# Kernel optimization log

Hardware: AMD Instinct MI355X
Metric: run time of the kernel (lower is better)

The kernel has to match this reference:

```python
import jax, jax.numpy as jnp
import numpy as np

EPS = 1e-5  # BatchNorm eps (ME.MinkowskiBatchNorm default)


def setup_inputs() -> dict:
    key = jax.random.key(0)
    k1, k2, k3, k4 = jax.random.split(key, 4)
    N, Cin, Cout, K = 65536, 256, 128, 8  # K = kernel_size**dimension = 2**3
    x = jax.random.normal(k1, (N, Cin), dtype=jnp.float32)
    W = jax.random.normal(k2, (K, Cin, Cout), dtype=jnp.float32) * 0.02
    gamma = jax.random.uniform(k3, (Cout,), dtype=jnp.float32, minval=0.5, maxval=1.5)
    beta = jax.random.normal(k4, (Cout,), dtype=jnp.float32) * 0.1
    return {"x": x, "W": W, "gamma": gamma, "beta": beta}


def reference(x, W, gamma, beta):
    # Transpose Minkowski conv, kernel=2, stride=2, dim=3: each input voxel
    # emits 2^3 = 8 disjoint child voxels; child for offset k gets x @ W[k].
    # Kernel map is identity per offset (no scatter-add collisions because
    # kernel_size == stride), so outputs stack to [8*N, Cout].
    Cout = W.shape[-1]
    out = jnp.einsum('nc,kcd->knd', x, W).reshape(-1, Cout)  # [8N, Cout]
    # MinkowskiBatchNorm over all active output sites (training batch stats).
    mean = jnp.mean(out, axis=0)
    var = jnp.mean(jnp.square(out - mean), axis=0)  # biased var, as BN uses
    y = (out - mean) * jax.lax.rsqrt(var + EPS) * gamma + beta
    return jnp.maximum(y, 0.0)  # MinkowskiReLU
```

## Files before the change

kernel.cpp:

```cpp
#include <hip/hip_runtime.h>
#include <stdint.h>

#define N_ROWS 65536
#define CIN 256
#define COUT 128

typedef __bf16 bf16x8 __attribute__((ext_vector_type(8)));
typedef float f32x4 __attribute__((ext_vector_type(4)));
typedef unsigned short u16;
typedef unsigned int u32;

__device__ __forceinline__ float truncbf(float f) {
  u32 x = __builtin_bit_cast(u32, f) & 0xFFFF0000u;
  return __builtin_bit_cast(float, x);
}
__device__ __forceinline__ u32 packbf(float a, float b) {
  return __builtin_amdgcn_perm(__builtin_bit_cast(u32, b),
                               __builtin_bit_cast(u32, a), 0x07060302u);
}

__device__ __forceinline__ void async_ld16(const void* g, void* l) {
  __builtin_amdgcn_global_load_lds((const __attribute__((address_space(1))) u32*)g,
                                   (__attribute__((address_space(3))) u32*)l,
                                   16, 0, 0);
}

template <bool EMIT_XB>
__global__ __launch_bounds__(512, 2) void gram_partial(const float* __restrict__ x,
                                                       float* __restrict__ part,
                                                       float* __restrict__ colsum,
                                                       u32* __restrict__ xb) {
  __shared__ u32 xT[256 * 18];
  __shared__ float cs_s[4][256];
  const int tid = threadIdx.x, lane = tid & 63;
  const int w = tid >> 6;
  const int wm = w >> 2, wn = w & 3;
  const int q = lane >> 4, r = lane & 15;
  const int row0 = blockIdx.x * 256;
  const int cpair = tid & 127, c0 = cpair * 2;
  const int npb = tid >> 7;

  f32x4 acc[8][4];
  #pragma unroll
  for (int i = 0; i < 8; ++i)
    #pragma unroll
    for (int j = 0; j < 4; ++j) acc[i][j] = (f32x4){0.f, 0.f, 0.f, 0.f};
  float cs0 = 0.f, cs1 = 0.f;

  for (int ch = 0; ch < 8; ++ch) {
    const int r0 = row0 + ch * 32;
    #pragma unroll
    for (int i = 0; i < 4; ++i) {
      int np = npb + i * 4;
      int n0 = r0 + np * 2;
      float2 g0 = *(const float2*)&x[(size_t)n0 * CIN + c0];
      float2 g1 = *(const float2*)&x[(size_t)(n0 + 1) * CIN + c0];
      xT[18 * c0 + np] = packbf(g0.x, g1.x);
      xT[18 * (c0 + 1) + np] = packbf(g0.y, g1.y);
      if (EMIT_XB) {
        xb[(size_t)n0 * 128 + cpair] = packbf(g0.x, g0.y);
        xb[(size_t)(n0 + 1) * 128 + cpair] = packbf(g1.x, g1.y);
      }
      cs0 += truncbf(g0.x) + truncbf(g1.x);
      cs1 += truncbf(g0.y) + truncbf(g1.y);
    }
    __syncthreads();
    bf16x8 af[8], bfr[4];
    #pragma unroll
    for (int mt = 0; mt < 8; ++mt) {
      int c = wm * 128 + mt * 16 + r;
      union { u32 d[4]; bf16x8 v; } t;
      const u32* p = &xT[18 * c + 4 * q];
      t.d[0] = p[0]; t.d[1] = p[1]; t.d[2] = p[2]; t.d[3] = p[3];
      af[mt] = t.v;
    }
    #pragma unroll
    for (int nt = 0; nt < 4; ++nt) {
      int c = wn * 64 + nt * 16 + r;
      union { u32 d[4]; bf16x8 v; } t;
      const u32* p = &xT[18 * c + 4 * q];
      t.d[0] = p[0]; t.d[1] = p[1]; t.d[2] = p[2]; t.d[3] = p[3];
      bfr[nt] = t.v;
    }
    #pragma unroll
    for (int mt = 0; mt < 8; ++mt)
      #pragma unroll
      for (int nt = 0; nt < 4; ++nt)
        acc[mt][nt] = __builtin_amdgcn_mfma_f32_16x16x32_bf16(af[mt], bfr[nt], acc[mt][nt], 0, 0, 0);
    __syncthreads();
  }

  float* pb = part + (size_t)blockIdx.x * 65536;
  #pragma unroll
  for (int mt = 0; mt < 8; ++mt)
    #pragma unroll
    for (int nt = 0; nt < 4; ++nt)
      #pragma unroll
      for (int i = 0; i < 4; ++i) {
        int row = wm * 128 + mt * 16 + q * 4 + i;
        int col = wn * 64 + nt * 16 + r;
        pb[row * 256 + col] = acc[mt][nt][i];
      }

  cs_s[npb][c0] = cs0;
  cs_s[npb][c0 + 1] = cs1;
  __syncthreads();
  if (tid < 256)
    atomicAdd(&colsum[tid], cs_s[0][tid] + cs_s[1][tid] + cs_s[2][tid] + cs_s[3][tid]);
}

__global__ void gram_reduce(const float* __restrict__ part, float* __restrict__ G) {
  int g = blockIdx.x * 256 + threadIdx.x;
  float s = 0.f;
  for (int b = 0; b < 256; ++b) s += part[(size_t)b * 65536 + g];
  G[g] = s;
}

__global__ __launch_bounds__(256) void stats_kernel(const float* __restrict__ G,
                                                    const float* __restrict__ colsum,
                                                    const float* __restrict__ W,
                                                    const float* __restrict__ gamma,
                                                    const float* __restrict__ beta,
                                                    float* __restrict__ scale,
                                                    float* __restrict__ bias) {
  const int d = blockIdx.x;
  const int t = threadIdx.x;
  __shared__ float wv[256][8];
  __shared__ float rr[16];
  float wt[8];
  #pragma unroll
  for (int k = 0; k < 8; ++k) wt[k] = truncbf(W[((size_t)k * CIN + t) * COUT + d]);
  #pragma unroll
  for (int k = 0; k < 8; ++k) wv[t][k] = wt[k];
  __syncthreads();

  float q = 0.f;
  for (int j = 0; j < 256; ++j) {
    float g = G[j * 256 + t];
    float dot = 0.f;
    #pragma unroll
    for (int k = 0; k < 8; ++k) dot += wv[j][k] * wt[k];
    q += g * dot;
  }
  float wsum = 0.f;
  #pragma unroll
  for (int k = 0; k < 8; ++k) wsum += wt[k];
  float m = colsum[t] * wsum;

  #pragma unroll
  for (int off = 32; off; off >>= 1) {
    q += __shfl_down(q, off, 64);
    m += __shfl_down(m, off, 64);
  }
  int wid = t >> 6;
  if ((t & 63) == 0) { rr[wid] = q; rr[wid + 8] = m; }
  __syncthreads();
  if (t == 0) {
    float qt = rr[0] + rr[1] + rr[2] + rr[3];
    float mn = rr[8] + rr[9] + rr[10] + rr[11];
    const float invM = 1.f / 524288.f;
    float mean = mn * invM;
    float var = qt * invM - mean * mean;
    float s = gamma[d] * rsqrtf(var + 1e-5f);
    scale[d] = s;
    bias[d] = beta[d] - mean * s;
  }
}

__global__ void wtrans_kernel(const float* __restrict__ W, u16* __restrict__ Wt) {
  __shared__ u16 tile[32][128];
  const int blk = blockIdx.x, t = threadIdx.x;
  const int k = blk >> 3, cb = blk & 7;
  #pragma unroll
  for (int i = 0; i < 4; ++i) {
    int u = t + i * 256;
    int ci = u >> 5, d4 = (u & 31) * 4;
    float4 f = *(const float4*)&W[((size_t)k * CIN + cb * 32 + ci) * COUT + d4];
    uint2 p; p.x = packbf(f.x, f.y); p.y = packbf(f.z, f.w);
    *(uint2*)&tile[ci][d4] = p;
  }
  __syncthreads();
  #pragma unroll
  for (int i = 0; i < 2; ++i) {
    int v = t + i * 256;
    int d = v >> 2, c0 = (v & 3) * 8;
    union { u16 s[8]; uint4 u4; } p;
    #pragma unroll
    for (int j = 0; j < 8; ++j) p.s[j] = tile[c0 + j][d];
    *(uint4*)&Wt[((size_t)blk * 128 + d) * 32 + c0] = p.u4;
  }
}

__global__ __launch_bounds__(256, 2) void gemm_xb(const u16* __restrict__ xb,
                                                  const u16* __restrict__ Wt,
                                                  const float* __restrict__ scale,
                                                  const float* __restrict__ bias,
                                                  float* __restrict__ out) {
  __shared__ u16 As[32768];
  const int tid = threadIdx.x, lane = tid & 63;
  const int w = tid >> 6, wr = w >> 1, wc = w & 1;
  const int q = lane >> 4, r = lane & 15;
  const int m0 = blockIdx.x * 128;

  #pragma unroll
  for (int i = 0; i < 16; ++i) {
    int u = tid + i * 256;
    int cb = u >> 9, row = (u >> 2) & 127, seg = u & 3;
    const u16* g = xb + (size_t)(m0 + row) * CIN + cb * 32 + seg * 8;
    async_ld16(g, As + (size_t)u * 8);
  }

  float sv[4], bv[4];
  #pragma unroll
  for (int nt = 0; nt < 4; ++nt) {
    int col = wc * 64 + nt * 16 + r;
    sv[nt] = scale[col]; bv[nt] = bias[col];
  }

  const int boff = (wc * 64 + r) * 32 + q * 8;
  bf16x8 bcur[4], bnext[4];
  #pragma unroll
  for (int nt = 0; nt < 4; ++nt)
    bcur[nt] = *(const bf16x8*)&Wt[boff + nt * 512];

  __syncthreads();

  int j = 0;
  for (int k = 0; k < 8; ++k) {
    f32x4 acc[4][4];
    #pragma unroll
    for (int i = 0; i < 4; ++i)
      #pragma unroll
      for (int jj = 0; jj < 4; ++jj) acc[i][jj] = (f32x4){0.f, 0.f, 0.f, 0.f};

    #pragma unroll
    for (int cb = 0; cb < 8; ++cb) {
      if (j < 63) {
        #pragma unroll
        for (int nt = 0; nt < 4; ++nt)
          bnext[nt] = *(const bf16x8*)&Wt[(size_t)(j + 1) * 4096 + boff + nt * 512];
      }
      bf16x8 af[4];
      #pragma unroll
      for (int mt = 0; mt < 4; ++mt)
        af[mt] = *(const bf16x8*)&As[((cb * 128) + wr * 64 + mt * 16 + r) * 32 + q * 8];
      #pragma unroll
      for (int mt = 0; mt < 4; ++mt)
        #pragma unroll
        for (int nt = 0; nt < 4; ++nt)
          acc[mt][nt] = __builtin_amdgcn_mfma_f32_16x16x32_bf16(af[mt], bcur[nt], acc[mt][nt], 0, 0, 0);
      if (j < 63) {
        #pragma unroll
        for (int nt = 0; nt < 4; ++nt) bcur[nt] = bnext[nt];
      }
      ++j;
    }

    const size_t obase = (size_t)k * N_ROWS + m0;
    #pragma unroll
    for (int mt = 0; mt < 4; ++mt)
      #pragma unroll
      for (int nt = 0; nt < 4; ++nt)
        #pragma unroll
        for (int i = 0; i < 4; ++i) {
          int grow = wr * 64 + mt * 16 + q * 4 + i;
          int col = wc * 64 + nt * 16 + r;
          float y = acc[mt][nt][i] * sv[nt] + bv[nt];
          y = y > 0.f ? y : 0.f;
          out[(obase + grow) * COUT + col] = y;
        }
  }
}

__global__ __launch_bounds__(256, 2) void gemm_fp32(const float* __restrict__ x,
                                                    const u16* __restrict__ Wt,
                                                    const float* __restrict__ scale,
                                                    const float* __restrict__ bias,
                                                    float* __restrict__ out) {
  __shared__ float Asf[4096];
  const int tid = threadIdx.x, lane = tid & 63;
  const int w = tid >> 6, wr = w >> 1, wc = w & 1;
  const int q = lane >> 4, r = lane & 15;
  const int k = blockIdx.x & 7;
  const int m0 = (blockIdx.x >> 3) * 128;

  const u16* wbase = Wt + (size_t)k * 8 * 4096;
  const int boff = (wc * 64 + r) * 32 + q * 8;

  bf16x8 bcur[4], bnext[4];
  #pragma unroll
  for (int nt = 0; nt < 4; ++nt)
    bcur[nt] = *(const bf16x8*)&wbase[boff + nt * 512];

  f32x4 acc[4][4];
  #pragma unroll
  for (int i = 0; i < 4; ++i)
    #pragma unroll
    for (int j = 0; j < 4; ++j) acc[i][j] = (f32x4){0.f, 0.f, 0.f, 0.f};

  for (int cb = 0; cb < 8; ++cb) {
    #pragma unroll
    for (int i = 0; i < 4; ++i) {
      int u = tid + i * 256;
      int row = u >> 3;
      int s = (u & 7) ^ (row & 7);
      const float* g = x + (size_t)(m0 + row) * CIN + cb * 32 + s * 4;
      async_ld16(g, Asf + (w * 64 + i * 256) * 4);
    }
    if (cb < 7) {
      #pragma unroll
      for (int nt = 0; nt < 4; ++nt)
        bnext[nt] = *(const bf16x8*)&wbase[(cb + 1) * 4096 + boff + nt * 512];
    }
    __syncthreads();
    bf16x8 af[4];
    #pragma unroll
    for (int mt = 0; mt < 4; ++mt) {
      int row = wr * 64 + mt * 16 + r;
      union { u32 d[4]; bf16x8 v; } t;
      #pragma unroll
      for (int b = 0; b < 2; ++b) {
        int unit = row * 8 + ((2 * q + b) ^ (row & 7));
        float4 f = *(const float4*)&Asf[unit * 4];
        t.d[b * 2 + 0] = packbf(f.x, f.y);
        t.d[b * 2 + 1] = packbf(f.z, f.w);
      }
      af[mt] = t.v;
    }
    #pragma unroll
    for (int mt = 0; mt < 4; ++mt)
      #pragma unroll
      for (int nt = 0; nt < 4; ++nt)
        acc[mt][nt] = __builtin_amdgcn_mfma_f32_16x16x32_bf16(af[mt], bcur[nt], acc[mt][nt], 0, 0, 0);
    __syncthreads();
    if (cb < 7) {
      #pragma unroll
      for (int nt = 0; nt < 4; ++nt) bcur[nt] = bnext[nt];
    }
  }

  float sv[4], bv[4];
  #pragma unroll
  for (int nt = 0; nt < 4; ++nt) {
    int col = wc * 64 + nt * 16 + r;
    sv[nt] = scale[col]; bv[nt] = bias[col];
  }
  const size_t obase = (size_t)k * N_ROWS + m0;
  #pragma unroll
  for (int mt = 0; mt < 4; ++mt)
    #pragma unroll
    for (int nt = 0; nt < 4; ++nt)
      #pragma unroll
      for (int i = 0; i < 4; ++i) {
        int grow = wr * 64 + mt * 16 + q * 4 + i;
        int col = wc * 64 + nt * 16 + r;
        float y = acc[mt][nt][i] * sv[nt] + bv[nt];
        y = y > 0.f ? y : 0.f;
        out[(obase + grow) * COUT + col] = y;
      }
}

extern "C" void kernel_launch(void* const* d_in, const int* in_sizes, int n_in,
                              void* d_out, int out_size, void* d_ws, size_t ws_size,
                              hipStream_t stream) {
  const float* x = (const float*)d_in[0];
  const float* W = (const float*)d_in[1];
  const float* gamma = (const float*)d_in[2];
  const float* beta = (const float*)d_in[3];
  float* out = (float*)d_out;

  float* ws = (float*)d_ws;
  float* G = ws;
  float* colsum = ws + 65536;
  float* scale = ws + 65792;
  float* bias = ws + 65920;
  u16* Wt = (u16*)(ws + 66048);
  u32* xb = (u32*)((char*)d_ws + (1 << 20));
  const size_t need = (1u << 20) + (size_t)N_ROWS * CIN * 2;
  const bool big_ws = ws_size >= need;

  float* part = (float*)d_out;

  hipMemsetAsync(colsum, 0, 256 * sizeof(float), stream);
  if (big_ws) {
    gram_partial<true><<<256, 512, 0, stream>>>(x, part, colsum, xb);
  } else {
    gram_partial<false><<<256, 512, 0, stream>>>(x, part, colsum, xb);
  }
  gram_reduce<<<256, 256, 0, stream>>>(part, G);
  stats_kernel<<<128, 256, 0, stream>>>(G, colsum, W, gamma, beta, scale, bias);
  wtrans_kernel<<<64, 256, 0, stream>>>(W, Wt);
  if (big_ws) {
    gemm_xb<<<512, 256, 0, stream>>>((const u16*)xb, Wt, scale, bias, out);
  } else {
    gemm_fp32<<<4096, 256, 0, stream>>>(x, Wt, scale, bias, out);
  }
}
```

Baseline: 392.6 us.

## Vectorize gram loads, swizzle GEMM LDS tile, widen gram reduce, drop colsum atomics

The Gram-partial kernel now reads x as float4 per thread and stores transposed bf16 pairs into a row-major LDS tile with padded stride, with wider xb stores. Per-block column sums are written to a buffer and summed in the stats kernel, which removes the atomics and the memset. gram_reduce is spread over 1024 blocks with float4 loads and an LDS tree. The GEMM A-tile gets an XOR swizzle to reduce LDS bank conflicts. The cost is a larger workspace offset and a serial 256-element loop per thread in stats.

Result: no change. 398.4 us (+1.5%).

```diff
diff --git a/kernel.cpp b/kernel.cpp
--- a/kernel.cpp
+++ b/kernel.cpp
@@ -28,41 +28,53 @@
 template <bool EMIT_XB>
 __global__ __launch_bounds__(512, 2) void gram_partial(const float* __restrict__ x,
                                                        float* __restrict__ part,
-                                                       float* __restrict__ colsum,
+                                                       float* __restrict__ csb,
                                                        u32* __restrict__ xb) {
-  __shared__ u32 xT[256 * 18];
-  __shared__ float cs_s[4][256];
+  __shared__ u32 xT[16 * 260];
+  __shared__ float cs_s[8][256];
   const int tid = threadIdx.x, lane = tid & 63;
   const int w = tid >> 6;
   const int wm = w >> 2, wn = w & 3;
   const int q = lane >> 4, r = lane & 15;
   const int row0 = blockIdx.x * 256;
-  const int cpair = tid & 127, c0 = cpair * 2;
-  const int npb = tid >> 7;
+  const int cq = tid & 63;
+  const int np2 = tid >> 6;
 
   f32x4 acc[8][4];
   #pragma unroll
   for (int i = 0; i < 8; ++i)
     #pragma unroll
     for (int j = 0; j < 4; ++j) acc[i][j] = (f32x4){0.f, 0.f, 0.f, 0.f};
-  float cs0 = 0.f, cs1 = 0.f;
+  f32x4 cs = (f32x4){0.f, 0.f, 0.f, 0.f};
 
   for (int ch = 0; ch < 8; ++ch) {
     const int r0 = row0 + ch * 32;
-    #pragma unroll
-    for (int i = 0; i < 4; ++i) {
-      int np = npb + i * 4;
-      int n0 = r0 + np * 2;
-      float2 g0 = *(const float2*)&x[(size_t)n0 * CIN + c0];
-      float2 g1 = *(const float2*)&x[(size_t)(n0 + 1) * CIN + c0];
-      xT[18 * c0 + np] = packbf(g0.x, g1.x);
-      xT[18 * (c0 + 1) + np] = packbf(g0.y, g1.y);
-      if (EMIT_XB) {
-        xb[(size_t)n0 * 128 + cpair] = packbf(g0.x, g0.y);
-        xb[(size_t)(n0 + 1) * 128 + cpair] = packbf(g1.x, g1.y);
-      }
-      cs0 += truncbf(g0.x) + truncbf(g1.x);
-      cs1 += truncbf(g0.y) + truncbf(g1.y);
+    const int nA = r0 + np2 * 2;
+    const int nB = r0 + (np2 + 8) * 2;
+    f32x4 a0 = *(const f32x4*)&x[(size_t)nA * CIN + 4 * cq];
+    f32x4 a1 = *(const f32x4*)&x[(size_t)(nA + 1) * CIN + 4 * cq];
+    f32x4 b0 = *(const f32x4*)&x[(size_t)nB * CIN + 4 * cq];
+    f32x4 b1 = *(const f32x4*)&x[(size_t)(nB + 1) * CIN + 4 * cq];
+
+    union { u32 d[4]; uint4 v; } pA, pB;
+    #pragma unroll
+    for (int j = 0; j < 4; ++j) {
+      pA.d[j] = packbf(a0[j], a1[j]);
+      pB.d[j] = packbf(b0[j], b1[j]);
+      cs[j] += truncbf(a0[j]) + truncbf(a1[j]) + truncbf(b0[j]) + truncbf(b1[j]);
+    }
+    *(uint4*)&xT[np2 * 260 + 4 * cq] = pA.v;
+    *(uint4*)&xT[(np2 + 8) * 260 + 4 * cq] = pB.v;
+    if (EMIT_XB) {
+      uint2 e;
+      e.x = packbf(a0[0], a0[1]); e.y = packbf(a0[2], a0[3]);
+      *(uint2*)&xb[(size_t)nA * 128 + 2 * cq] = e;
+      e.x = packbf(a1[0], a1[1]); e.y = packbf(a1[2], a1[3]);
+      *(uint2*)&xb[(size_t)(nA + 1) * 128 + 2 * cq] = e;
+      e.x = packbf(b0[0], b0[1]); e.y = packbf(b0[2], b0[3]);
+      *(uint2*)&xb[(size_t)nB * 128 + 2 * cq] = e;
+      e.x = packbf(b1[0], b1[1]); e.y = packbf(b1[2], b1[3]);
+      *(uint2*)&xb[(size_t)(nB + 1) * 128 + 2 * cq] = e;
     }
     __syncthreads();
     bf16x8 af[8], bfr[4];
@@ -70,16 +82,16 @@
     for (int mt = 0; mt < 8; ++mt) {
       int c = wm * 128 + mt * 16 + r;
       union { u32 d[4]; bf16x8 v; } t;
-      const u32* p = &xT[18 * c + 4 * q];
-      t.d[0] = p[0]; t.d[1] = p[1]; t.d[2] = p[2]; t.d[3] = p[3];
+      #pragma unroll
+      for (int s = 0; s < 4; ++s) t.d[s] = xT[(4 * q + s) * 260 + c];
       af[mt] = t.v;
     }
     #pragma unroll
     for (int nt = 0; nt < 4; ++nt) {
       int c = wn * 64 + nt * 16 + r;
       union { u32 d[4]; bf16x8 v; } t;
-      const u32* p = &xT[18 * c + 4 * q];
-      t.d[0] = p[0]; t.d[1] = p[1]; t.d[2] = p[2]; t.d[3] = p[3];
+      #pragma unroll
+      for (int s = 0; s < 4; ++s) t.d[s] = xT[(4 * q + s) * 260 + c];
       bfr[nt] = t.v;
     }
     #pragma unroll
@@ -102,22 +114,38 @@
         pb[row * 256 + col] = acc[mt][nt][i];
       }
 
-  cs_s[npb][c0] = cs0;
-  cs_s[npb][c0 + 1] = cs1;
-  __syncthreads();
-  if (tid < 256)
-    atomicAdd(&colsum[tid], cs_s[0][tid] + cs_s[1][tid] + cs_s[2][tid] + cs_s[3][tid]);
-}
-
-__global__ void gram_reduce(const float* __restrict__ part, float* __restrict__ G) {
-  int g = blockIdx.x * 256 + threadIdx.x;
-  float s = 0.f;
-  for (int b = 0; b < 256; ++b) s += part[(size_t)b * 65536 + g];
-  G[g] = s;
+  *(f32x4*)&cs_s[np2][4 * cq] = cs;
+  __syncthreads();
+  if (tid < 256) {
+    float s = 0.f;
+    #pragma unroll
+    for (int p = 0; p < 8; ++p) s += cs_s[p][tid];
+    csb[(size_t)blockIdx.x * 256 + tid] = s;
+  }
+}
+
+__global__ __launch_bounds__(256) void gram_reduce(const float* __restrict__ part,
+                                                   float* __restrict__ G) {
+  __shared__ float red[16][64];
+  const int t = threadIdx.x;
+  const int fi = t & 15, grp = t >> 4;
+  const int g0 = blockIdx.x * 64;
+  f32x4 a = (f32x4){0.f, 0.f, 0.f, 0.f};
+  const float* p = part + (size_t)(grp * 16) * 65536 + g0 + fi * 4;
+  #pragma unroll
+  for (int b = 0; b < 16; ++b) a += *(const f32x4*)(p + (size_t)b * 65536);
+  *(f32x4*)&red[grp][fi * 4] = a;
+  __syncthreads();
+  if (t < 64) {
+    float s = 0.f;
+    #pragma unroll
+    for (int gq = 0; gq < 16; ++gq) s += red[gq][t];
+    G[g0 + t] = s;
+  }
 }
 
 __global__ __launch_bounds__(256) void stats_kernel(const float* __restrict__ G,
-                                                    const float* __restrict__ colsum,
+                                                    const float* __restrict__ csb,
                                                     const float* __restrict__ W,
                                                     const float* __restrict__ gamma,
                                                     const float* __restrict__ beta,
@@ -127,6 +155,8 @@
   const int t = threadIdx.x;
   __shared__ float wv[256][8];
   __shared__ float rr[16];
+  float cst = 0.f;
+  for (int b = 0; b < 256; ++b) cst += csb[b * 256 + t];
   float wt[8];
   #pragma unroll
   for (int k = 0; k < 8; ++k) wt[k] = truncbf(W[((size_t)k * CIN + t) * COUT + d]);
@@ -145,7 +175,7 @@
   float wsum = 0.f;
   #pragma unroll
   for (int k = 0; k < 8; ++k) wsum += wt[k];
-  float m = colsum[t] * wsum;
+  float m = cst * wsum;
 
   #pragma unroll
   for (int off = 32; off; off >>= 1) {
@@ -205,8 +235,9 @@
   #pragma unroll
   for (int i = 0; i < 16; ++i) {
     int u = tid + i * 256;
-    int cb = u >> 9, row = (u >> 2) & 127, seg = u & 3;
-    const u16* g = xb + (size_t)(m0 + row) * CIN + cb * 32 + seg * 8;
+    int cb = u >> 9, row = (u >> 2) & 127;
+    int sseg = (u ^ (u >> 3)) & 3;
+    const u16* g = xb + (size_t)(m0 + row) * CIN + cb * 32 + sseg * 8;
     async_ld16(g, As + (size_t)u * 8);
   }
 
@@ -218,6 +249,7 @@
   }
 
   const int boff = (wc * 64 + r) * 32 + q * 8;
+  const int sw = (q ^ ((r >> 1) & 3)) * 8;
   bf16x8 bcur[4], bnext[4];
   #pragma unroll
   for (int nt = 0; nt < 4; ++nt)
@@ -243,7 +275,7 @@
       bf16x8 af[4];
       #pragma unroll
       for (int mt = 0; mt < 4; ++mt)
-        af[mt] = *(const bf16x8*)&As[((cb * 128) + wr * 64 + mt * 16 + r) * 32 + q * 8];
+        af[mt] = *(const bf16x8*)&As[((cb * 128) + wr * 64 + mt * 16 + r) * 32 + sw];
       #pragma unroll
       for (int mt = 0; mt < 4; ++mt)
         #pragma unroll
@@ -371,24 +403,23 @@
 
   float* ws = (float*)d_ws;
   float* G = ws;
-  float* colsum = ws + 65536;
-  float* scale = ws + 65792;
-  float* bias = ws + 65920;
-  u16* Wt = (u16*)(ws + 66048);
-  u32* xb = (u32*)((char*)d_ws + (1 << 20));
-  const size_t need = (1u << 20) + (size_t)N_ROWS * CIN * 2;
+  float* csb = ws + 65536;
+  float* scale = ws + 131072;
+  float* bias = ws + 131200;
+  u16* Wt = (u16*)(ws + 131328);
+  u32* xb = (u32*)((char*)d_ws + (2u << 20));
+  const size_t need = (2u << 20) + (size_t)N_ROWS * CIN * 2;
   const bool big_ws = ws_size >= need;
 
   float* part = (float*)d_out;
 
-  hipMemsetAsync(colsum, 0, 256 * sizeof(float), stream);
   if (big_ws) {
-    gram_partial<true><<<256, 512, 0, stream>>>(x, part, colsum, xb);
+    gram_partial<true><<<256, 512, 0, stream>>>(x, part, csb, xb);
   } else {
-    gram_partial<false><<<256, 512, 0, stream>>>(x, part, colsum, xb);
-  }
-  gram_reduce<<<256, 256, 0, stream>>>(part, G);
-  stats_kernel<<<128, 256, 0, stream>>>(G, colsum, W, gamma, beta, scale, bias);
+    gram_partial<false><<<256, 512, 0, stream>>>(x, part, csb, xb);
+  }
+  gram_reduce<<<1024, 256, 0, stream>>>(part, G);
+  stats_kernel<<<128, 256, 0, stream>>>(G, csb, W, gamma, beta, scale, bias);
   wtrans_kernel<<<64, 256, 0, stream>>>(W, Wt);
   if (big_ws) {
     gemm_xb<<<512, 256, 0, stream>>>((const u16*)xb, Wt, scale, bias, out);
```
